# Kernel optimization log

Hardware: AMD Instinct MI355X
Metric: run time of the kernel (lower is better)

Reference implementation:

```python
import jax, jax.numpy as jnp
import numpy as np

D_MODEL = 1024
N_HEADS = 16
D_K = D_MODEL // N_HEADS  # 64, also d_v
B, S = 8, 1024


def setup_inputs() -> dict:
    key = jax.random.key(0)
    ks = jax.random.split(key, 12)
    sc = 1.0 / np.sqrt(D_MODEL)
    inp = {
        "q": jax.random.normal(ks[0], (B, S, D_MODEL), jnp.float32),
        "k": jax.random.normal(ks[1], (B, S, D_MODEL), jnp.float32),
        "v": jax.random.normal(ks[2], (B, S, D_MODEL), jnp.float32),
        # per-head projection weights stacked over heads; torch Linear stores [out,in]
        "Wq": jax.random.normal(ks[3], (N_HEADS, D_K, D_MODEL), jnp.float32) * sc,
        "bq": jax.random.normal(ks[4], (N_HEADS, D_K), jnp.float32) * sc,
        "Wk": jax.random.normal(ks[5], (N_HEADS, D_K, D_MODEL), jnp.float32) * sc,
        "bk": jax.random.normal(ks[6], (N_HEADS, D_K), jnp.float32) * sc,
        "Wv": jax.random.normal(ks[7], (N_HEADS, D_K, D_MODEL), jnp.float32) * sc,
        "bv": jax.random.normal(ks[8], (N_HEADS, D_K), jnp.float32) * sc,
        "Wf": jax.random.normal(ks[9], (D_MODEL, D_MODEL), jnp.float32) * sc,
        "bf": jax.random.normal(ks[10], (D_MODEL,), jnp.float32) * sc,
    }
    return inp


def reference(q, k, v, Wq, bq, Wk, bk, Wv, bv, Wf, bf):
    temper = jnp.asarray(D_K ** 0.5, q.dtype)
    # per-head linear projections, all heads at once: [b,s,h,dk]
    qh = jnp.einsum('bsd,hkd->bhsk', q, Wq) + bq[None, :, None, :]
    kh = jnp.einsum('bsd,hkd->bhsk', k, Wk) + bk[None, :, None, :]
    vh = jnp.einsum('bsd,hkd->bhsk', v, Wv) + bv[None, :, None, :]
    # scaled dot-product scores [b,h,s,s]
    scores = jnp.einsum('bhik,bhjk->bhij', qh, kh) / temper
    # faithful scalar-equality mask: positions exactly equal to mask (=0) -> -inf
    scores = jnp.where(scores == 0.0, -jnp.inf, scores)
    attn = jax.nn.softmax(scores, axis=-1)
    out = jnp.einsum('bhij,bhjv->bhiv', attn, vh)  # [b,h,s,dv]
    # concat heads (head order matches torch.cat over ModuleList)
    out = out.transpose(0, 2, 1, 3).reshape(out.shape[0], out.shape[2], -1)  # [b,s,d_model]
    return out @ Wf.T + bf
```

## Files before the change

kernel.cpp:

```cpp
#include <hip/hip_runtime.h>
#include <hip/hip_bf16.h>


#define D_MODEL_ 1024
#define NH_ 16
#define DK_ 64
#define B_ 8
#define S_ 1024
#define M_ (B_ * S_)

typedef __hip_bfloat16 bf16;
typedef __attribute__((ext_vector_type(8))) short short8;
typedef __attribute__((ext_vector_type(4))) short short4_t;
typedef __attribute__((ext_vector_type(4))) float f32x4;

typedef const __attribute__((address_space(1))) unsigned int* gas_u32p;
typedef __attribute__((address_space(3))) unsigned int* las_u32p;

__device__ __forceinline__ short f2bs(float x) {
  bf16 h = __float2bfloat16(x);
  return *reinterpret_cast<short*>(&h);
}

__global__ __launch_bounds__(256)
void conv_w4(const float* __restrict__ w0, const float* __restrict__ w1,
             const float* __restrict__ w2, const float* __restrict__ w3,
             bf16* __restrict__ out) {
  const float* src = (blockIdx.z == 0) ? w0 : (blockIdx.z == 1) ? w1
                   : (blockIdx.z == 2) ? w2 : w3;
  size_t i = ((size_t)blockIdx.x * 256 + threadIdx.x) * 8;
  f32x4 a = *(const f32x4*)(src + i);
  f32x4 b = *(const f32x4*)(src + i + 4);
  short8 s;
  s[0] = f2bs(a[0]); s[1] = f2bs(a[1]); s[2] = f2bs(a[2]); s[3] = f2bs(a[3]);
  s[4] = f2bs(b[0]); s[5] = f2bs(b[1]); s[6] = f2bs(b[2]); s[7] = f2bs(b[3]);
  *(short8*)((short*)out + (size_t)blockIdx.z * 1024 * 1024 + i) = s;
}

template<int BN, int AF32>
__device__ __forceinline__ void gemm_body(const void* __restrict__ A,
                                          const bf16* __restrict__ Wb,
                                          const float* __restrict__ bias,
                                          void* __restrict__ C,
                                          int cMode, float cscale, int m0, int n0)
{
  __shared__ short As[2][128 * 32];
  __shared__ short Bs[2][BN * 32];
  const int tid = threadIdx.x;
  const int lane = tid & 63;
  const int w = tid >> 6;
  const int l15 = lane & 15, quad = lane >> 4;
  const int wm = (w >> 1) * 64, wn = (w & 1) * (BN / 2);
  const int srow = lane >> 2;
  const int sslot = ((lane & 3) ^ ((lane >> 3) & 3)) * 8;
  const int rsl = (quad ^ ((l15 >> 1) & 3)) * 8;

  f32x4 au[4], av[4];
  auto loadAf = [&](int k0) {
    const float* Af = (const float*)A;
#pragma unroll
    for (int p = 0; p < 4; ++p) {
      int c = p * 256 + tid;
      int r = c >> 3, kc = (c & 7) * 8;
      const float* g = Af + (size_t)(m0 + r) * 1024 + k0 + kc;
      au[p] = *(const f32x4*)g;
      av[p] = *(const f32x4*)(g + 4);
    }
  };
  auto writeAf = [&]() {
#pragma unroll
    for (int p = 0; p < 4; ++p) {
      int c = p * 256 + tid;
      int r = c >> 3, kc = (c & 7) * 8;
      int s = (c & 3) ^ ((r >> 1) & 3);
      short8 sv;
      sv[0] = f2bs(au[p][0]); sv[1] = f2bs(au[p][1]); sv[2] = f2bs(au[p][2]); sv[3] = f2bs(au[p][3]);
      sv[4] = f2bs(av[p][0]); sv[5] = f2bs(av[p][1]); sv[6] = f2bs(av[p][2]); sv[7] = f2bs(av[p][3]);
      *(short8*)&As[kc >> 5][r * 32 + s * 8] = sv;
    }
  };

  f32x4 acc[4][BN / 32];
#pragma unroll
  for (int i = 0; i < 4; ++i)
#pragma unroll
    for (int j = 0; j < BN / 32; ++j)
      acc[i][j] = (f32x4){0.f, 0.f, 0.f, 0.f};

  if (AF32) loadAf(0);

  for (int k0 = 0; k0 < 1024; k0 += 64) {
    __syncthreads();
    if (AF32) {
      writeAf();
    } else {
      const bf16* Ab = (const bf16*)A;
#pragma unroll
      for (int sub = 0; sub < 2; ++sub)
#pragma unroll
        for (int p = 0; p < 2; ++p) {
          int r = 32 * w + 16 * p + srow;
          __builtin_amdgcn_global_load_lds(
              (gas_u32p)(const void*)(Ab + (size_t)(m0 + r) * 1024 + k0 + sub * 32 + sslot),
              (las_u32p)(void*)((char*)&As[sub][0] + w * 2048 + p * 1024), 16, 0, 0);
        }
    }
#pragma unroll
    for (int sub = 0; sub < 2; ++sub)
#pragma unroll
      for (int p = 0; p < BN / 64; ++p) {
        int r = (BN / 4) * w + 16 * p + srow;
        __builtin_amdgcn_global_load_lds(
            (gas_u32p)(const void*)(Wb + (size_t)(n0 + r) * 1024 + k0 + sub * 32 + sslot),
            (las_u32p)(void*)((char*)&Bs[sub][0] + w * (BN / 4) * 64 + p * 1024), 16, 0, 0);
      }
    __syncthreads();

    if (AF32 && k0 + 64 < 1024) loadAf(k0 + 64);

#pragma unroll
    for (int kk = 0; kk < 2; ++kk) {
      short8 af[4], bfv[BN / 32];
#pragma unroll
      for (int t = 0; t < 4; ++t)
        af[t]  = *(short8*)&As[kk][(wm + t * 16 + l15) * 32 + rsl];
#pragma unroll
      for (int t = 0; t < BN / 32; ++t)
        bfv[t] = *(short8*)&Bs[kk][(wn + t * 16 + l15) * 32 + rsl];
#pragma unroll
      for (int mt = 0; mt < 4; ++mt)
#pragma unroll
        for (int nt = 0; nt < BN / 32; ++nt)
          acc[mt][nt] = __builtin_amdgcn_mfma_f32_16x16x32_bf16(af[mt], bfv[nt], acc[mt][nt], 0, 0, 0);
    }
  }

  if (cMode == 2) {
    bf16* vt = (bf16*)C;
    const int bidx = m0 >> 10;
    const int sbase = (m0 & 1023) + wm;
#pragma unroll
    for (int nt = 0; nt < BN / 32; ++nt) {
      int n = n0 + wn + nt * 16 + l15;
      float bv = bias[n];
#pragma unroll
      for (int mt = 0; mt < 4; ++mt) {
        int s = sbase + mt * 16 + quad * 4;
        short4_t pk;
#pragma unroll
        for (int r = 0; r < 4; ++r) pk[r] = f2bs((acc[mt][nt][r] + bv) * cscale);
        *(short4_t*)((short*)vt + ((size_t)bidx * 1024 + n) * 1024 + s) = pk;
      }
    }
  } else {
#pragma unroll
    for (int nt = 0; nt < BN / 32; ++nt) {
      int col = n0 + wn + nt * 16 + l15;
      float bv = bias[col];
#pragma unroll
      for (int mt = 0; mt < 4; ++mt)
#pragma unroll
        for (int r = 0; r < 4; ++r) {
          int row = m0 + wm + mt * 16 + quad * 4 + r;
          float val = (acc[mt][nt][r] + bv) * cscale;
          if (cMode == 1) ((float*)C)[(size_t)row * 1024 + col] = val;
          else ((bf16*)C)[(size_t)row * 1024 + col] = __float2bfloat16(val);
        }
    }
  }
}

__global__ __launch_bounds__(256)
void gemm_proj(const float* __restrict__ q, const float* __restrict__ k,
               const float* __restrict__ v, const bf16* __restrict__ wq,
               const bf16* __restrict__ wk, const bf16* __restrict__ wv,
               const float* __restrict__ bq, const float* __restrict__ bk,
               const float* __restrict__ bv, void* __restrict__ cq,
               void* __restrict__ ck, void* __restrict__ cv)
{
  const int z = blockIdx.z;
  const float* A = (z == 0) ? q : (z == 1) ? k : v;
  const bf16* W  = (z == 0) ? wq : (z == 1) ? wk : wv;
  const float* bb = (z == 0) ? bq : (z == 1) ? bk : bv;
  void* C = (z == 0) ? cq : (z == 1) ? ck : cv;
  int cMode = (z == 2) ? 2 : 0;
  float cscale = (z == 0) ? 0.18033688011112042f : 1.0f;
  gemm_body<128, 1>(A, W, bb, C, cMode, cscale, blockIdx.x * 128, blockIdx.y * 128);
}

__global__ __launch_bounds__(256)
void gemm_final(const bf16* __restrict__ A, const bf16* __restrict__ W,
                const float* __restrict__ bias, void* __restrict__ C)
{
  gemm_body<64, 0>(A, W, bias, C, 1, 1.0f, blockIdx.x * 128, blockIdx.y * 64);
}

__global__ __launch_bounds__(512)
void attn_mfma(const bf16* __restrict__ QH, const bf16* __restrict__ KH,
               const bf16* __restrict__ VT, bf16* __restrict__ AO)
{
  __shared__ short Ks[2][64 * 32];
  __shared__ short Vs[2][64 * 32];
  __shared__ short Ps[8][16 * 72];
  const int tid = threadIdx.x;
  const int lane = tid & 63;
  const int w = tid >> 6;
  const int l15 = lane & 15, quad = lane >> 4;
  const int q0 = blockIdx.x * 128;
  const int h = blockIdx.y, b = blockIdx.z;
  const size_t base = ((size_t)b * S_) * D_MODEL_ + (size_t)h * DK_;
  const size_t vtb  = (((size_t)b * NH_ + h) * DK_) * (size_t)S_;
  const float NEG = -1e30f;
  const float THR = 11.54156032f;
  short* myPs = Ps[w];

  const int sw = w & 3;
  const int srow = sw * 16 + (lane >> 2);
  const int sslot = ((lane & 3) ^ ((lane >> 3) & 3)) * 8;
  const int rsl = (quad ^ ((l15 >> 1) & 3)) * 8;

  short8 qa[2];
#pragma unroll
  for (int ks = 0; ks < 2; ++ks)
    qa[ks] = *(const short8*)((const short*)QH + base + (size_t)(q0 + w * 16 + l15) * D_MODEL_ + ks * 32 + quad * 8);

  float mi = NEG, li = 0.f;
  f32x4 oacc[4];
#pragma unroll
  for (int nt = 0; nt < 4; ++nt) oacc[nt] = (f32x4){0.f, 0.f, 0.f, 0.f};

  for (int j0 = 0; j0 < S_; j0 += 64) {
    __syncthreads();
    if (w < 4) {
#pragma unroll
      for (int sub = 0; sub < 2; ++sub)
        __builtin_amdgcn_global_load_lds(
            (gas_u32p)(const void*)((const short*)KH + base + (size_t)(j0 + srow) * D_MODEL_ + sub * 32 + sslot),
            (las_u32p)(void*)((char*)&Ks[sub][0] + sw * 1024), 16, 0, 0);
    } else {
#pragma unroll
      for (int sub = 0; sub < 2; ++sub)
        __builtin_amdgcn_global_load_lds(
            (gas_u32p)(const void*)((const short*)VT + vtb + (size_t)srow * S_ + j0 + sub * 32 + sslot),
            (las_u32p)(void*)((char*)&Vs[sub][0] + sw * 1024), 16, 0, 0);
    }
    __syncthreads();

    short8 kb[4][2], vb[4][2];
#pragma unroll
    for (int nt = 0; nt < 4; ++nt)
#pragma unroll
      for (int ks = 0; ks < 2; ++ks) {
        kb[nt][ks] = *(short8*)&Ks[ks][(nt * 16 + l15) * 32 + rsl];
        vb[nt][ks] = *(short8*)&Vs[ks][(nt * 16 + l15) * 32 + rsl];
      }

    f32x4 sacc[4];
#pragma unroll
    for (int nt = 0; nt < 4; ++nt) sacc[nt] = (f32x4){0.f, 0.f, 0.f, 0.f};
    __builtin_amdgcn_s_setprio(1);
#pragma unroll
    for (int nt = 0; nt < 4; ++nt)
#pragma unroll
      for (int ks = 0; ks < 2; ++ks)
        sacc[nt] = __builtin_amdgcn_mfma_f32_16x16x32_bf16(kb[nt][ks], qa[ks], sacc[nt], 0, 0, 0);
    __builtin_amdgcn_s_setprio(0);

    float p[4][4];
#pragma unroll
    for (int nt = 0; nt < 4; ++nt)
#pragma unroll
      for (int r = 0; r < 4; ++r) {
        float x = sacc[nt][r];
        if (x == 0.0f) x = NEG;
        p[nt][r] = x;
      }
    float mm[4];
#pragma unroll
    for (int nt = 0; nt < 4; ++nt)
      mm[nt] = fmaxf(fmaxf(p[nt][0], p[nt][1]), fmaxf(p[nt][2], p[nt][3]));
    float rm = fmaxf(fmaxf(mm[0], mm[1]), fmaxf(mm[2], mm[3]));
    rm = fmaxf(rm, __shfl_xor(rm, 16, 64));
    rm = fmaxf(rm, __shfl_xor(rm, 32, 64));

    const bool skip = __all(rm <= mi + THR);
    const float nm = skip ? mi : fmaxf(mi, rm);

    float psum[4];
#pragma unroll
    for (int nt = 0; nt < 4; ++nt) {
      float e0 = exp2f(p[nt][0] - nm), e1 = exp2f(p[nt][1] - nm);
      float e2 = exp2f(p[nt][2] - nm), e3 = exp2f(p[nt][3] - nm);
      p[nt][0] = e0; p[nt][1] = e1; p[nt][2] = e2; p[nt][3] = e3;
      psum[nt] = (e0 + e1) + (e2 + e3);
    }
    float ps = (psum[0] + psum[1]) + (psum[2] + psum[3]);
    ps += __shfl_xor(ps, 16, 64);
    ps += __shfl_xor(ps, 32, 64);

    if (skip) {
      li += ps;
    } else {
      float alpha = exp2f(mi - nm);
      li = li * alpha + ps;
      float ar[4];
#pragma unroll
      for (int r = 0; r < 4; ++r) ar[r] = __shfl(alpha, quad * 4 + r, 64);
#pragma unroll
      for (int nt = 0; nt < 4; ++nt)
#pragma unroll
        for (int r = 0; r < 4; ++r) oacc[nt][r] *= ar[r];
    }
    mi = nm;

#pragma unroll
    for (int nt = 0; nt < 4; ++nt) {
      short4_t pk;
#pragma unroll
      for (int r = 0; r < 4; ++r) pk[r] = f2bs(p[nt][r]);
      *(short4_t*)&myPs[l15 * 72 + nt * 16 + quad * 4] = pk;
    }

    __threadfence_block();

    short8 pa[2];
#pragma unroll
    for (int ks = 0; ks < 2; ++ks)
      pa[ks] = *(short8*)&myPs[l15 * 72 + ks * 32 + quad * 8];
    __builtin_amdgcn_s_setprio(1);
#pragma unroll
    for (int nt = 0; nt < 4; ++nt)
#pragma unroll
      for (int ks = 0; ks < 2; ++ks)
        oacc[nt] = __builtin_amdgcn_mfma_f32_16x16x32_bf16(pa[ks], vb[nt][ks], oacc[nt], 0, 0, 0);
    __builtin_amdgcn_s_setprio(0);
  }

  float lr[4];
#pragma unroll
  for (int r = 0; r < 4; ++r) lr[r] = __shfl(li, quad * 4 + r, 64);
#pragma unroll
  for (int r = 0; r < 4; ++r) {
    float inv = (lr[r] > 0.f) ? 1.0f / lr[r] : 0.f;
    int q = q0 + w * 16 + quad * 4 + r;
#pragma unroll
    for (int nt = 0; nt < 4; ++nt)
      AO[base + (size_t)q * D_MODEL_ + nt * 16 + l15] = __float2bfloat16(oacc[nt][r] * inv);
  }
}

extern "C" void kernel_launch(void* const* d_in, const int* in_sizes, int n_in,
                              void* d_out, int out_size, void* d_ws, size_t ws_size,
                              hipStream_t stream) {
  (void)in_sizes; (void)n_in; (void)out_size;
  const float* q  = (const float*)d_in[0];
  const float* k  = (const float*)d_in[1];
  const float* v  = (const float*)d_in[2];
  const float* Wq = (const float*)d_in[3];
  const float* bq = (const float*)d_in[4];
  const float* Wk = (const float*)d_in[5];
  const float* bk = (const float*)d_in[6];
  const float* Wv = (const float*)d_in[7];
  const float* bv = (const float*)d_in[8];
  const float* Wf = (const float*)d_in[9];
  const float* bF = (const float*)d_in[10];

  const size_t MB = (size_t)1024 * 1024;
  char* ws = (char*)d_ws;
  bf16* wqb = (bf16*)(ws);
  bf16* wkb = (bf16*)(ws + 2 * MB);
  bf16* wvb = (bf16*)(ws + 4 * MB);
  bf16* wfb = (bf16*)(ws + 6 * MB);
  bf16* vt  = (bf16*)(ws + 8 * MB);
  bf16* qh  = (bf16*)d_out;
  bf16* kh  = (bf16*)((char*)d_out + 16 * MB);

  const bool bigws = ws_size >= (size_t)40 * MB;
  bf16* aob = bigws ? (bf16*)(ws + 24 * MB) : qh;
  bf16* fin = bigws ? aob : (bf16*)(ws + 8 * MB);

  dim3 blk(256);

  conv_w4<<<dim3(512, 1, 4), blk, 0, stream>>>(Wq, Wk, Wv, Wf, wqb);

  gemm_proj<<<dim3(M_ / 128, D_MODEL_ / 128, 3), blk, 0, stream>>>(
      q, k, v, wqb, wkb, wvb, bq, bk, bv, qh, kh, vt);

  attn_mfma<<<dim3(S_ / 128, NH_, B_), dim3(512), 0, stream>>>(qh, kh, vt, aob);

  if (!bigws)
    hipMemcpyAsync(ws + 8 * MB, d_out, 16 * MB, hipMemcpyDeviceToDevice, stream);

  gemm_final<<<dim3(M_ / 128, D_MODEL_ / 64), blk, 0, stream>>>(fin, wfb, bF, d_out);
}
```

Measured before the change: 335.4 us.

## Stage K/V in two large 512-key chunks to cut attention barriers

The attention kernel now loads half of the sequence's K and V tiles (8 tiles of 64 keys) into LDS at once, then processes them without per-tile barriers. This replaces the two barriers per 64-key tile with four barriers in total. LDS use grows to about 130 KB per block, which reduces occupancy, and nothing overlaps the chunk loads with compute. The projection GEMM also issues the weight tile loads before the A-tile loads in each k-step.

```diff
diff --git a/kernel.cpp b/kernel.cpp
--- a/kernel.cpp
+++ b/kernel.cpp
@@ -91,6 +91,16 @@
 
   for (int k0 = 0; k0 < 1024; k0 += 64) {
     __syncthreads();
+
+#pragma unroll
+    for (int sub = 0; sub < 2; ++sub)
+#pragma unroll
+      for (int p = 0; p < BN / 64; ++p) {
+        int r = (BN / 4) * w + 16 * p + srow;
+        __builtin_amdgcn_global_load_lds(
+            (gas_u32p)(const void*)(Wb + (size_t)(n0 + r) * 1024 + k0 + sub * 32 + sslot),
+            (las_u32p)(void*)((char*)&Bs[sub][0] + w * (BN / 4) * 64 + p * 1024), 16, 0, 0);
+      }
     if (AF32) {
       writeAf();
     } else {
@@ -105,15 +115,6 @@
               (las_u32p)(void*)((char*)&As[sub][0] + w * 2048 + p * 1024), 16, 0, 0);
         }
     }
-#pragma unroll
-    for (int sub = 0; sub < 2; ++sub)
-#pragma unroll
-      for (int p = 0; p < BN / 64; ++p) {
-        int r = (BN / 4) * w + 16 * p + srow;
-        __builtin_amdgcn_global_load_lds(
-            (gas_u32p)(const void*)(Wb + (size_t)(n0 + r) * 1024 + k0 + sub * 32 + sslot),
-            (las_u32p)(void*)((char*)&Bs[sub][0] + w * (BN / 4) * 64 + p * 1024), 16, 0, 0);
-      }
     __syncthreads();
 
     if (AF32 && k0 + 64 < 1024) loadAf(k0 + 64);
@@ -199,8 +200,8 @@
 void attn_mfma(const bf16* __restrict__ QH, const bf16* __restrict__ KH,
                const bf16* __restrict__ VT, bf16* __restrict__ AO)
 {
-  __shared__ short Ks[2][64 * 32];
-  __shared__ short Vs[2][64 * 32];
+  __shared__ short Ks[8][2][64 * 32];
+  __shared__ short Vs[8][2][64 * 32];
   __shared__ short Ps[8][16 * 72];
   const int tid = threadIdx.x;
   const int lane = tid & 63;
@@ -219,6 +220,27 @@
   const int sslot = ((lane & 3) ^ ((lane >> 3) & 3)) * 8;
   const int rsl = (quad ^ ((l15 >> 1) & 3)) * 8;
 
+  auto stage_chunk = [&](int c) {
+    const int sb = c * 512;
+    if (w < 4) {
+#pragma unroll
+      for (int jt = 0; jt < 8; ++jt)
+#pragma unroll
+        for (int sub = 0; sub < 2; ++sub)
+          __builtin_amdgcn_global_load_lds(
+              (gas_u32p)(const void*)((const short*)KH + base + (size_t)(sb + jt * 64 + srow) * D_MODEL_ + sub * 32 + sslot),
+              (las_u32p)(void*)((char*)&Ks[jt][sub][0] + sw * 1024), 16, 0, 0);
+    } else {
+#pragma unroll
+      for (int jt = 0; jt < 8; ++jt)
+#pragma unroll
+        for (int sub = 0; sub < 2; ++sub)
+          __builtin_amdgcn_global_load_lds(
+              (gas_u32p)(const void*)((const short*)VT + vtb + (size_t)srow * S_ + sb + jt * 64 + sub * 32 + sslot),
+              (las_u32p)(void*)((char*)&Vs[jt][sub][0] + sw * 1024), 16, 0, 0);
+    }
+  };
+
   short8 qa[2];
 #pragma unroll
   for (int ks = 0; ks < 2; ++ks)
@@ -229,30 +251,14 @@
 #pragma unroll
   for (int nt = 0; nt < 4; ++nt) oacc[nt] = (f32x4){0.f, 0.f, 0.f, 0.f};
 
-  for (int j0 = 0; j0 < S_; j0 += 64) {
-    __syncthreads();
-    if (w < 4) {
-#pragma unroll
-      for (int sub = 0; sub < 2; ++sub)
-        __builtin_amdgcn_global_load_lds(
-            (gas_u32p)(const void*)((const short*)KH + base + (size_t)(j0 + srow) * D_MODEL_ + sub * 32 + sslot),
-            (las_u32p)(void*)((char*)&Ks[sub][0] + sw * 1024), 16, 0, 0);
-    } else {
-#pragma unroll
-      for (int sub = 0; sub < 2; ++sub)
-        __builtin_amdgcn_global_load_lds(
-            (gas_u32p)(const void*)((const short*)VT + vtb + (size_t)srow * S_ + j0 + sub * 32 + sslot),
-            (las_u32p)(void*)((char*)&Vs[sub][0] + sw * 1024), 16, 0, 0);
-    }
-    __syncthreads();
-
+  auto process = [&](int jt) {
     short8 kb[4][2], vb[4][2];
 #pragma unroll
     for (int nt = 0; nt < 4; ++nt)
 #pragma unroll
       for (int ks = 0; ks < 2; ++ks) {
-        kb[nt][ks] = *(short8*)&Ks[ks][(nt * 16 + l15) * 32 + rsl];
-        vb[nt][ks] = *(short8*)&Vs[ks][(nt * 16 + l15) * 32 + rsl];
+        kb[nt][ks] = *(short8*)&Ks[jt][ks][(nt * 16 + l15) * 32 + rsl];
+        vb[nt][ks] = *(short8*)&Vs[jt][ks][(nt * 16 + l15) * 32 + rsl];
       }
 
     f32x4 sacc[4];
@@ -334,7 +340,18 @@
       for (int ks = 0; ks < 2; ++ks)
         oacc[nt] = __builtin_amdgcn_mfma_f32_16x16x32_bf16(pa[ks], vb[nt][ks], oacc[nt], 0, 0, 0);
     __builtin_amdgcn_s_setprio(0);
-  }
+  };
+
+  stage_chunk(0);
+  __syncthreads();
+#pragma unroll 2
+  for (int jt = 0; jt < 8; ++jt) process(jt);
+
+  __syncthreads();
+  stage_chunk(1);
+  __syncthreads();
+#pragma unroll 2
+  for (int jt = 0; jt < 8; ++jt) process(jt);
 
   float lr[4];
 #pragma unroll
```

Result: slower. 360.6 us (+7.5%).
